# Optimization experiments

Measured on AMD Instinct MI355X. Metric: run time of the kernel, lower is better.

Reference implementation:

```python
import jax, jax.numpy as jnp
import numpy as np

D_MODEL = 1024
N_HEADS = 16
HEAD_DIM = D_MODEL // N_HEADS
LN_EPS = 1e-5


def _linear_init(key, fan_in, fan_out):
    # xavier_uniform for weight, zeros for bias; torch Linear weight is [out, in]
    limit = float(np.sqrt(6.0 / (fan_in + fan_out)))
    w = jax.random.uniform(key, (fan_out, fan_in), jnp.float32, -limit, limit)
    b = jnp.zeros((fan_out,), jnp.float32)
    return w, b


def setup_inputs() -> dict:
    key = jax.random.key(0)
    ks = jax.random.split(key, 8)
    B, S, D = 4, 1024, D_MODEL
    query = jax.random.normal(ks[0], (B, S, D), jnp.float32)
    key_t = jax.random.normal(ks[1], (B, S, D), jnp.float32)
    value = jax.random.normal(ks[2], (B, S, D), jnp.float32)
    Wq, bq = _linear_init(ks[3], D, D)
    Wk, bk = _linear_init(ks[4], D, D)
    Wv, bv = _linear_init(ks[5], D, D)
    Wfq, bfq = _linear_init(ks[6], D, D)
    Wfk, bfk = _linear_init(ks[7], D, D)
    gamma_q = jnp.ones((D,), jnp.float32); beta_q = jnp.zeros((D,), jnp.float32)
    gamma_k = jnp.ones((D,), jnp.float32); beta_k = jnp.zeros((D,), jnp.float32)
    return {"query": query, "key": key_t, "value": value,
            "Wq": Wq, "bq": bq, "Wk": Wk, "bk": bk, "Wv": Wv, "bv": bv,
            "Wfq": Wfq, "bfq": bfq, "Wfk": Wfk, "bfk": bfk,
            "gamma_q": gamma_q, "beta_q": beta_q,
            "gamma_k": gamma_k, "beta_k": beta_k}


def _layernorm(x, gamma, beta):
    mu = jnp.mean(x, axis=-1, keepdims=True)
    var = jnp.mean(jnp.square(x - mu), axis=-1, keepdims=True)
    return (x - mu) * jax.lax.rsqrt(var + LN_EPS) * gamma + beta


def reference(query, key, value, Wq, bq, Wk, bk, Wv, bv, Wfq, bfq, Wfk, bfk,
              gamma_q, beta_q, gamma_k, beta_k):
    B, Sq, D = query.shape
    H, Hd = N_HEADS, HEAD_DIM
    scale = jnp.sqrt(jnp.asarray(Hd, jnp.float32))

    residual_q, residual_k = query, key
    # torch Linear: x @ W.T + b
    q = (query @ Wq.T + bq).reshape(B, Sq, H, Hd).transpose(0, 2, 1, 3)  # [B,H,Sq,Hd]
    k = (key @ Wk.T + bk).reshape(B, -1, H, Hd).transpose(0, 2, 1, 3)    # [B,H,Sk,Hd]
    v = (value @ Wv.T + bv).reshape(B, -1, H, Hd).transpose(0, 2, 1, 3)  # [B,H,Sv,Hd]

    # Q->K attention (dropout disabled / eval mode)
    energy = jnp.einsum('bhqd,bhkd->bhqk', q, k) / scale
    attn_q2k = jax.nn.softmax(energy, axis=-1)
    x_q = jnp.einsum('bhqk,bhkd->bhqd', attn_q2k, v)
    x_q = x_q.transpose(0, 2, 1, 3).reshape(B, Sq, D)

    # K->Q attention (shares V)
    energy_k = jnp.einsum('bhkd,bhqd->bhkq', k, q) / scale
    attn_k2q = jax.nn.softmax(energy_k, axis=-1)
    x_k = jnp.einsum('bhkq,bhqd->bhkd', attn_k2q, v)
    x_k = x_k.transpose(0, 2, 1, 3).reshape(B, -1, D)

    q_out = x_q @ Wfq.T + bfq
    query_out = _layernorm(residual_q + q_out, gamma_q, beta_q)
    k_out = x_k @ Wfk.T + bfk
    key_out = _layernorm(residual_k + k_out, gamma_k, beta_k)
    return (query_out, key_out)
```

## Files before the change

kernel.cpp:

```cpp
#include <hip/hip_runtime.h>

typedef unsigned short u16;
typedef unsigned int u32;
typedef __attribute__((ext_vector_type(8))) short short8;
typedef __attribute__((ext_vector_type(4))) float floatx4;
typedef __attribute__((ext_vector_type(16))) float f32x16;

#define AS_GLOBAL __attribute__((address_space(1)))
#define AS_LDS    __attribute__((address_space(3)))

__device__ __forceinline__ float b2f(u16 v) {
  union { u32 u; float f; } x; x.u = ((u32)v) << 16; return x.f;
}
__device__ __forceinline__ u16 f2bf(float f) {
  union { float f; u32 u; } x; x.f = f;
  u32 r = (x.u + 0x7fffu + ((x.u >> 16) & 1u)) >> 16;
  return (u16)r;
}
__device__ __forceinline__ void gl_lds16(const u16* g, u16* l) {
  __builtin_amdgcn_global_load_lds((const AS_GLOBAL u32*)g, (AS_LDS u32*)l, 16, 0, 0);
}

__global__ __launch_bounds__(256)
void cvt8(const float* __restrict__ s0, const float* __restrict__ s1, const float* __restrict__ s2,
          const float* __restrict__ s3, const float* __restrict__ s4, const float* __restrict__ s5,
          const float* __restrict__ s6, const float* __restrict__ s7,
          u16* __restrict__ d0, u16* __restrict__ d1, u16* __restrict__ d2,
          u16* __restrict__ d3, u16* __restrict__ d4, u16* __restrict__ d5,
          u16* __restrict__ d6, u16* __restrict__ d7, int nbig, int nsmall)
{
  const int z = blockIdx.y;
  const float* s; u16* d; int n;
  switch (z) {
    case 0: s = s0; d = d0; n = nbig; break;
    case 1: s = s1; d = d1; n = nbig; break;
    case 2: s = s2; d = d2; n = nbig; break;
    case 3: s = s3; d = d3; n = nsmall; break;
    case 4: s = s4; d = d4; n = nsmall; break;
    case 5: s = s5; d = d5; n = nsmall; break;
    case 6: s = s6; d = d6; n = nsmall; break;
    default: s = s7; d = d7; n = nsmall; break;
  }
  const size_t idx = ((size_t)blockIdx.x * 256 + threadIdx.x) * 8;
  if (idx >= (size_t)n) return;
  float4 a0 = *(const float4*)(s + idx);
  float4 a1 = *(const float4*)(s + idx + 4);
  u16 t[8];
  t[0] = f2bf(a0.x); t[1] = f2bf(a0.y); t[2] = f2bf(a0.z); t[3] = f2bf(a0.w);
  t[4] = f2bf(a1.x); t[5] = f2bf(a1.y); t[6] = f2bf(a1.z); t[7] = f2bf(a1.w);
  *(uint4*)(d + idx) = *(const uint4*)t;
}

template <int TRANS2>
__global__ __launch_bounds__(256, 3)
void gemm_nt_bias(const u16* __restrict__ A0, const u16* __restrict__ W0, const float* __restrict__ B0, u16* __restrict__ C0,
                  const u16* __restrict__ A1, const u16* __restrict__ W1, const float* __restrict__ B1, u16* __restrict__ C1,
                  const u16* __restrict__ A2, const u16* __restrict__ W2, const float* __restrict__ B2, u16* __restrict__ C2)
{
  constexpr int K = 1024, N = 1024;
  __shared__ __attribute__((aligned(16))) u16 As[128 * 64];
  __shared__ __attribute__((aligned(16))) u16 Bs[128 * 64];

  const int z = blockIdx.z;
  const u16*   A  = z == 0 ? A0 : (z == 1 ? A1 : A2);
  const u16*   W  = z == 0 ? W0 : (z == 1 ? W1 : W2);
  const float* Bi = z == 0 ? B0 : (z == 1 ? B1 : B2);
  u16*         C  = z == 0 ? C0 : (z == 1 ? C1 : C2);

  const int tid  = threadIdx.x;
  const int lane = tid & 63;
  const int wave = tid >> 6;
  const int l16  = lane & 15;
  const int quad = lane >> 4;
  const int wm = wave >> 1, wn = wave & 1;
  const int m0 = blockIdx.x * 128;
  const int n0 = blockIdx.y * 128;

  floatx4 acc[4][4];
#pragma unroll
  for (int i = 0; i < 4; ++i)
#pragma unroll
    for (int j = 0; j < 4; ++j)
#pragma unroll
      for (int e = 0; e < 4; ++e) acc[i][j][e] = 0.f;

  const int srow = wave * 32 + (lane >> 3);
  const int scol = (lane & 7) * 8;
  const u16* gA = A + (size_t)(m0 + srow) * K + scol;
  const u16* gW = W + (size_t)(n0 + srow) * K + scol;

  for (int k0 = 0; k0 < K; k0 += 64) {
#pragma unroll
    for (int i = 0; i < 4; ++i) {
      gl_lds16(gA + (size_t)(i * 8) * K + k0, &As[(wave * 32 + i * 8) * 64]);
      gl_lds16(gW + (size_t)(i * 8) * K + k0, &Bs[(wave * 32 + i * 8) * 64]);
    }
    __syncthreads();
#pragma unroll
    for (int ks = 0; ks < 2; ++ks) {
      short8 af[4], bf[4];
#pragma unroll
      for (int mt = 0; mt < 4; ++mt)
        af[mt] = *(const short8*)&As[(wm * 64 + mt * 16 + l16) * 64 + ks * 32 + quad * 8];
#pragma unroll
      for (int nt = 0; nt < 4; ++nt)
        bf[nt] = *(const short8*)&Bs[(wn * 64 + nt * 16 + l16) * 64 + ks * 32 + quad * 8];
#pragma unroll
      for (int mt = 0; mt < 4; ++mt)
#pragma unroll
        for (int nt = 0; nt < 4; ++nt)
          acc[mt][nt] = __builtin_amdgcn_mfma_f32_16x16x32_bf16(af[mt], bf[nt], acc[mt][nt], 0, 0, 0);
    }
    __syncthreads();
  }

  float bb[4];
#pragma unroll
  for (int nt = 0; nt < 4; ++nt) bb[nt] = Bi[n0 + wn * 64 + nt * 16 + l16];

  if (TRANS2 && z == 2) {
#pragma unroll
    for (int mt = 0; mt < 4; ++mt) {
      const int rowb = m0 + wm * 64 + mt * 16 + quad * 4;
#pragma unroll
      for (int nt = 0; nt < 4; ++nt) {
        const int col = n0 + wn * 64 + nt * 16 + l16;
        u32 lo = (u32)f2bf(acc[mt][nt][0] + bb[nt]) | ((u32)f2bf(acc[mt][nt][1] + bb[nt]) << 16);
        u32 hi = (u32)f2bf(acc[mt][nt][2] + bb[nt]) | ((u32)f2bf(acc[mt][nt][3] + bb[nt]) << 16);
        uint2 w; w.x = lo; w.y = hi;
        *(uint2*)&C[(size_t)col * 4096 + rowb] = w;
      }
    }
  } else {
#pragma unroll
    for (int mt = 0; mt < 4; ++mt) {
#pragma unroll
      for (int r = 0; r < 4; ++r) {
        const int row = m0 + wm * 64 + mt * 16 + quad * 4 + r;
        u16* crow = C + (size_t)row * N + n0 + wn * 64 + l16;
#pragma unroll
        for (int nt = 0; nt < 4; ++nt)
          crow[nt * 16] = f2bf(acc[mt][nt][r] + bb[nt]);
      }
    }
  }
}

__global__ __launch_bounds__(256, 3)
void flash32(const u16* __restrict__ Qg, const u16* __restrict__ Kg,
             const u16* __restrict__ VTw, u16* __restrict__ OQ, u16* __restrict__ OK)
{
  __shared__ __attribute__((aligned(16))) u16 smem[4 * 4096];
  __shared__ __attribute__((aligned(16))) u16 pbuf[4][32 * 64];

  const int tid = threadIdx.x;
  const int lane = tid & 63;
  const int wave = tid >> 6;
  const int l32 = lane & 31;
  const int hi = lane >> 5;
  const int b = blockIdx.y >> 4, h = blockIdx.y & 15;
  const int q0 = blockIdx.x * 128;

  const u16* Qw = blockIdx.z ? Kg : Qg;
  const u16* Kw = blockIdx.z ? Qg : Kg;
  u16* Ow = blockIdx.z ? OK : OQ;

  const int rr = lane >> 3;
  const int s7 = lane & 7;

  const u16* Qt = Qw + ((size_t)(b * 1024 + q0)) * 1024 + h * 64;
  const u16* Kt = Kw + ((size_t)(b * 1024)) * 1024 + h * 64;
  const u16* Vt = VTw + ((size_t)(h * 64)) * 4096 + (size_t)b * 1024;

#pragma unroll
  for (int c = 0; c < 4; ++c) {
    const int R = wave * 32 + c * 8;
    const int cg = ((s7 ^ rr ^ (R >> 3)) & 7) << 3;
    gl_lds16(Qt + (size_t)(R + rr) * 1024 + cg, smem + (R < 64 ? 4096 : 8192) + R * 64);
  }
  {
    u16* kd = smem + wave * 1024;
    u16* vd = smem + 8192 + wave * 1024;
    const int R0 = wave * 16, R1 = wave * 16 + 8;
    const int cg0 = ((s7 ^ rr ^ (R0 >> 3)) & 7) << 3;
    const int cg1 = ((s7 ^ rr ^ (R1 >> 3)) & 7) << 3;
    gl_lds16(Kt + (size_t)(R0 + rr) * 1024 + cg0, kd);
    gl_lds16(Kt + (size_t)(R1 + rr) * 1024 + cg1, kd + 512);
    gl_lds16(Vt + (size_t)(R0 + rr) * 4096 + cg0, vd);
    gl_lds16(Vt + (size_t)(R1 + rr) * 4096 + cg1, vd + 512);
  }
  __syncthreads();

  const int qr = wave * 32 + l32;
  const int qkey = (qr ^ (qr >> 3)) & 7;
  const u16* qbase = smem + (wave < 2 ? 4096 : 8192) + qr * 64;
  short8 aq[4];
#pragma unroll
  for (int d2 = 0; d2 < 4; ++d2)
    aq[d2] = *(const short8*)(qbase + (((d2 * 2 + hi) ^ qkey) & 7) * 8);
  __syncthreads();

  const int key0 = (l32 ^ (l32 >> 3)) & 7;
  const int key1 = key0 ^ 4;

  f32x16 accO0, accO1;
#pragma unroll
  for (int i = 0; i < 16; ++i) { accO0[i] = 0.f; accO1[i] = 0.f; }
  float m = -1e30f, lsum = 0.f;
  const float scale = 0.125f;
  u16* pb = pbuf[wave];

  for (int jt = 0; jt < 16; ++jt) {
    const int cur = jt & 1;
    const u16* ksb = smem + cur * 4096;
    const u16* vtb = smem + 8192 + cur * 4096;

    if (jt + 1 < 16) {
      const int nb = cur ^ 1;
      u16* kd = smem + nb * 4096 + wave * 1024;
      u16* vd = smem + 8192 + nb * 4096 + wave * 1024;
      const int R0 = wave * 16, R1 = wave * 16 + 8;
      const int cg0 = ((s7 ^ rr ^ (R0 >> 3)) & 7) << 3;
      const int cg1 = ((s7 ^ rr ^ (R1 >> 3)) & 7) << 3;
      const size_t tkn = (size_t)((jt + 1) * 64);
      gl_lds16(Kt + (tkn + R0 + rr) * 1024 + cg0, kd);
      gl_lds16(Kt + (tkn + R1 + rr) * 1024 + cg1, kd + 512);
      gl_lds16(Vt + (size_t)(R0 + rr) * 4096 + tkn + cg0, vd);
      gl_lds16(Vt + (size_t)(R1 + rr) * 4096 + tkn + cg1, vd + 512);
    }

    f32x16 s0, s1;
#pragma unroll
    for (int i = 0; i < 16; ++i) { s0[i] = 0.f; s1[i] = 0.f; }
#pragma unroll
    for (int d2 = 0; d2 < 4; ++d2) {
      const int g = d2 * 2 + hi;
      short8 k0 = *(const short8*)(ksb + l32 * 64 + ((g ^ key0) & 7) * 8);
      short8 k1 = *(const short8*)(ksb + (32 + l32) * 64 + ((g ^ key1) & 7) * 8);
      s0 = __builtin_amdgcn_mfma_f32_32x32x16_bf16(k0, aq[d2], s0, 0, 0, 0);
      s1 = __builtin_amdgcn_mfma_f32_32x32x16_bf16(k1, aq[d2], s1, 0, 0, 0);
    }

#define MAX8(v, o) fmaxf(fmaxf(fmaxf(v[o], v[o + 1]), fmaxf(v[o + 2], v[o + 3])), \
                         fmaxf(fmaxf(v[o + 4], v[o + 5]), fmaxf(v[o + 6], v[o + 7])))
#define SUM8(v, o) (((v[o] + v[o + 1]) + (v[o + 2] + v[o + 3])) + \
                    ((v[o + 4] + v[o + 5]) + (v[o + 6] + v[o + 7])))
    float mx = fmaxf(fmaxf(MAX8(s0, 0), MAX8(s0, 8)), fmaxf(MAX8(s1, 0), MAX8(s1, 8)));
    mx = fmaxf(mx, __shfl_xor(mx, 32, 64));
    const float mnew = fmaxf(m, mx * scale);
    const float alpha = __expf(m - mnew);
    m = mnew;
#pragma unroll
    for (int i = 0; i < 16; ++i) s0[i] = __expf(fmaf(s0[i], scale, -mnew));
#pragma unroll
    for (int i = 0; i < 16; ++i) s1[i] = __expf(fmaf(s1[i], scale, -mnew));
    float ssum = (SUM8(s0, 0) + SUM8(s0, 8)) + (SUM8(s1, 0) + SUM8(s1, 8));
    ssum += __shfl_xor(ssum, 32, 64);
    lsum = lsum * alpha + ssum;
#pragma unroll
    for (int i = 0; i < 16; ++i) { accO0[i] *= alpha; accO1[i] *= alpha; }

#define PWRITE(SV, KB)                                                         \
  _Pragma("unroll") for (int rq = 0; rq < 4; ++rq) {                           \
    const int g = (KB) * 4 + rq;                                               \
    uint2 w;                                                                   \
    w.x = (u32)f2bf(SV[rq * 4 + 0]) | ((u32)f2bf(SV[rq * 4 + 1]) << 16);       \
    w.y = (u32)f2bf(SV[rq * 4 + 2]) | ((u32)f2bf(SV[rq * 4 + 3]) << 16);       \
    *(uint2*)&pb[l32 * 64 + ((g ^ key0) & 7) * 8 + hi * 4] = w;                \
  }
    PWRITE(s0, 0)
    PWRITE(s1, 1)
#undef PWRITE

#pragma unroll
    for (int ks = 0; ks < 4; ++ks) {
      const int g = ks * 2 + hi;
      short8 v0 = *(const short8*)(vtb + l32 * 64 + ((g ^ key0) & 7) * 8);
      short8 v1 = *(const short8*)(vtb + (32 + l32) * 64 + ((g ^ key1) & 7) * 8);
      short8 pf = *(const short8*)&pb[l32 * 64 + ((g ^ key0) & 7) * 8];
      accO0 = __builtin_amdgcn_mfma_f32_32x32x16_bf16(v0, pf, accO0, 0, 0, 0);
      accO1 = __builtin_amdgcn_mfma_f32_32x32x16_bf16(v1, pf, accO1, 0, 0, 0);
    }
#undef MAX8
#undef SUM8
    __syncthreads();
  }

  const float invl = 1.f / lsum;
  u16* orow = Ow + ((size_t)(b * 1024 + q0 + wave * 32 + l32)) * 1024 + h * 64 + hi * 4;
#pragma unroll
  for (int rg = 0; rg < 4; ++rg) {
    uint2 w0, w1;
    w0.x = (u32)f2bf(accO0[rg * 4 + 0] * invl) | ((u32)f2bf(accO0[rg * 4 + 1] * invl) << 16);
    w0.y = (u32)f2bf(accO0[rg * 4 + 2] * invl) | ((u32)f2bf(accO0[rg * 4 + 3] * invl) << 16);
    *(uint2*)(orow + rg * 8) = w0;
    w1.x = (u32)f2bf(accO1[rg * 4 + 0] * invl) | ((u32)f2bf(accO1[rg * 4 + 1] * invl) << 16);
    w1.y = (u32)f2bf(accO1[rg * 4 + 2] * invl) | ((u32)f2bf(accO1[rg * 4 + 3] * invl) << 16);
    *(uint2*)(orow + 32 + rg * 8) = w1;
  }
}

__global__ __launch_bounds__(256)
void ln_residual(const u16* __restrict__ TQ, const u16* __restrict__ TK,
                 const float* __restrict__ Rq, const float* __restrict__ Rk,
                 const float* __restrict__ gq, const float* __restrict__ bq,
                 const float* __restrict__ gk, const float* __restrict__ bk,
                 float* __restrict__ out)
{
  const int row = blockIdx.x;
  const u16 *X; const float *R, *G, *Bt; float* O;
  if (row < 4096) {
    X = TQ + (size_t)row * 1024; R = Rq + (size_t)row * 1024;
    G = gq; Bt = bq; O = out + (size_t)row * 1024;
  } else {
    const int r2 = row - 4096;
    X = TK + (size_t)r2 * 1024; R = Rk + (size_t)r2 * 1024;
    G = gk; Bt = bk; O = out + (size_t)4096 * 1024 + (size_t)r2 * 1024;
  }
  const int tid = threadIdx.x;
  float v[4], sum = 0.f, sumsq = 0.f;
#pragma unroll
  for (int i = 0; i < 4; ++i) {
    const int c = tid + i * 256;
    const float x = b2f(X[c]) + R[c];
    v[i] = x; sum += x; sumsq += x * x;
  }
#pragma unroll
  for (int sh = 1; sh < 64; sh <<= 1) {
    sum += __shfl_xor(sum, sh, 64);
    sumsq += __shfl_xor(sumsq, sh, 64);
  }
  __shared__ float sm[8];
  const int wave = tid >> 6, lane = tid & 63;
  if (lane == 0) { sm[wave] = sum; sm[4 + wave] = sumsq; }
  __syncthreads();
  sum = sm[0] + sm[1] + sm[2] + sm[3];
  sumsq = sm[4] + sm[5] + sm[6] + sm[7];
  const float mu = sum * (1.f / 1024.f);
  const float var = sumsq * (1.f / 1024.f) - mu * mu;
  const float rstd = rsqrtf(var + 1e-5f);
#pragma unroll
  for (int i = 0; i < 4; ++i) {
    const int c = tid + i * 256;
    O[c] = (v[i] - mu) * rstd * G[c] + Bt[c];
  }
}

extern "C" void kernel_launch(void* const* d_in, const int* in_sizes, int n_in,
                              void* d_out, int out_size, void* d_ws, size_t ws_size,
                              hipStream_t stream)
{
  const float* query = (const float*)d_in[0];
  const float* key   = (const float*)d_in[1];
  const float* value = (const float*)d_in[2];
  const float* Wq  = (const float*)d_in[3];  const float* bq  = (const float*)d_in[4];
  const float* Wk  = (const float*)d_in[5];  const float* bk  = (const float*)d_in[6];
  const float* Wv  = (const float*)d_in[7];  const float* bv  = (const float*)d_in[8];
  const float* Wfq = (const float*)d_in[9];  const float* bfq = (const float*)d_in[10];
  const float* Wfk = (const float*)d_in[11]; const float* bfk = (const float*)d_in[12];
  const float* gq = (const float*)d_in[13];  const float* betaq = (const float*)d_in[14];
  const float* gk = (const float*)d_in[15];  const float* betak = (const float*)d_in[16];
  float* out = (float*)d_out;
  u16* ws  = (u16*)d_ws;

  const size_t SZ = (size_t)4096 * 1024;
  const size_t WZ = (size_t)1024 * 1024;
  u16* Qb  = ws;
  u16* Kb  = ws + SZ;
  u16* VT  = ws + 2 * SZ;
  u16* Wqb = ws + 3 * SZ;
  u16* Wkb = Wqb + WZ;
  u16* Wvb = Wkb + WZ;
  u16* Wfqb = Wvb + WZ;
  u16* Wfkb = Wfqb + WZ;
  u16* qbf = (u16*)out;
  u16* kbf = qbf + SZ;
  u16* vbf = kbf + SZ;
  u16* XQ = (u16*)out;
  u16* XK = (u16*)out + SZ;
  u16* TQ = Qb;
  u16* TK = Kb;

  cvt8<<<dim3(2048, 8), 256, 0, stream>>>(query, key, value, Wq, Wk, Wv, Wfq, Wfk,
                                          qbf, kbf, vbf, Wqb, Wkb, Wvb, Wfqb, Wfkb,
                                          (int)SZ, (int)WZ);
  gemm_nt_bias<1><<<dim3(32, 8, 3), 256, 0, stream>>>(qbf, Wqb, bq, Qb,
                                                      kbf, Wkb, bk, Kb,
                                                      vbf, Wvb, bv, VT);
  flash32<<<dim3(8, 64, 2), 256, 0, stream>>>(Qb, Kb, VT, XQ, XK);
  gemm_nt_bias<0><<<dim3(32, 8, 2), 256, 0, stream>>>(XQ, Wfqb, bfq, TQ,
                                                      XK, Wfkb, bfk, TK,
                                                      XK, Wfkb, bfk, TK);
  ln_residual<<<dim3(8192), 256, 0, stream>>>(TQ, TK, query, key,
                                              gq, betaq, gk, betak, out);
}
```

Baseline: 283.8 us.

## Rework flash attention softmax: exp2, lazy rescale, split P buffer, occupancy 4

The flash attention kernel gets several changes at once. It uses exp2 with a folded log2e scale and skips the output rescale when the running max grows by less than a threshold. The P tile is written and consumed in two 32-column halves, which halves the P buffer in LDS. It also raises the launch bound to 4 blocks per SM, adds s_setprio around the MFMA blocks, uses packed bf16 conversion intrinsics, and remaps block indices so neighbouring blocks are spread across heads and batches. The aim is less VALU and LDS pressure and higher occupancy, at the risk of register spilling under the tighter bound.

```diff
diff --git a/kernel.cpp b/kernel.cpp
--- a/kernel.cpp
+++ b/kernel.cpp
@@ -1,4 +1,5 @@
 #include <hip/hip_runtime.h>
+#include <hip/hip_bf16.h>
 
 typedef unsigned short u16;
 typedef unsigned int u32;
@@ -16,6 +17,10 @@
   union { float f; u32 u; } x; x.f = f;
   u32 r = (x.u + 0x7fffu + ((x.u >> 16) & 1u)) >> 16;
   return (u16)r;
+}
+__device__ __forceinline__ u32 pk2(float lo, float hi) {
+  __hip_bfloat162 h = __float22bfloat162_rn(make_float2(lo, hi));
+  u32 r; __builtin_memcpy(&r, &h, 4); return r;
 }
 __device__ __forceinline__ void gl_lds16(const u16* g, u16* l) {
   __builtin_amdgcn_global_load_lds((const AS_GLOBAL u32*)g, (AS_LDS u32*)l, 16, 0, 0);
@@ -146,24 +151,30 @@
   }
 }
 
-__global__ __launch_bounds__(256, 3)
+__global__ __launch_bounds__(256, 4)
 void flash32(const u16* __restrict__ Qg, const u16* __restrict__ Kg,
              const u16* __restrict__ VTw, u16* __restrict__ OQ, u16* __restrict__ OK)
 {
   __shared__ __attribute__((aligned(16))) u16 smem[4 * 4096];
-  __shared__ __attribute__((aligned(16))) u16 pbuf[4][32 * 64];
+  __shared__ __attribute__((aligned(16))) u16 pbuf[4][32 * 32];
 
   const int tid = threadIdx.x;
   const int lane = tid & 63;
   const int wave = tid >> 6;
   const int l32 = lane & 31;
   const int hi = lane >> 5;
-  const int b = blockIdx.y >> 4, h = blockIdx.y & 15;
-  const int q0 = blockIdx.x * 128;
-
-  const u16* Qw = blockIdx.z ? Kg : Qg;
-  const u16* Kw = blockIdx.z ? Qg : Kg;
-  u16* Ow = blockIdx.z ? OK : OQ;
+
+  const int jlin = blockIdx.x + 8 * (blockIdx.y + 64 * blockIdx.z);
+  const int L = (jlin & 7) * 128 + (jlin >> 3);
+  const int qx = L & 7;
+  const int by = (L >> 3) & 63;
+  const int bz = L >> 9;
+  const int b = by >> 4, h = by & 15;
+  const int q0 = qx * 128;
+
+  const u16* Qw = bz ? Kg : Qg;
+  const u16* Kw = bz ? Qg : Kg;
+  u16* Ow = bz ? OK : OQ;
 
   const int rr = lane >> 3;
   const int s7 = lane & 7;
@@ -202,13 +213,14 @@
 
   const int key0 = (l32 ^ (l32 >> 3)) & 7;
   const int key1 = key0 ^ 4;
+  const int kq = (l32 >> 2) & 3;
+  u16* pb = pbuf[wave];
 
   f32x16 accO0, accO1;
 #pragma unroll
   for (int i = 0; i < 16; ++i) { accO0[i] = 0.f; accO1[i] = 0.f; }
-  float m = -1e30f, lsum = 0.f;
-  const float scale = 0.125f;
-  u16* pb = pbuf[wave];
+  float m2 = -1e30f, lsum = 0.f;
+  const float SCL2 = 0.18033688011112042f;
 
   for (int jt = 0; jt < 16; ++jt) {
     const int cur = jt & 1;
@@ -232,6 +244,7 @@
     f32x16 s0, s1;
 #pragma unroll
     for (int i = 0; i < 16; ++i) { s0[i] = 0.f; s1[i] = 0.f; }
+    __builtin_amdgcn_s_setprio(1);
 #pragma unroll
     for (int d2 = 0; d2 < 4; ++d2) {
       const int g = d2 * 2 + hi;
@@ -240,6 +253,7 @@
       s0 = __builtin_amdgcn_mfma_f32_32x32x16_bf16(k0, aq[d2], s0, 0, 0, 0);
       s1 = __builtin_amdgcn_mfma_f32_32x32x16_bf16(k1, aq[d2], s1, 0, 0, 0);
     }
+    __builtin_amdgcn_s_setprio(0);
 
 #define MAX8(v, o) fmaxf(fmaxf(fmaxf(v[o], v[o + 1]), fmaxf(v[o + 2], v[o + 3])), \
                          fmaxf(fmaxf(v[o + 4], v[o + 5]), fmaxf(v[o + 6], v[o + 7])))
@@ -247,42 +261,45 @@
                     ((v[o + 4] + v[o + 5]) + (v[o + 6] + v[o + 7])))
     float mx = fmaxf(fmaxf(MAX8(s0, 0), MAX8(s0, 8)), fmaxf(MAX8(s1, 0), MAX8(s1, 8)));
     mx = fmaxf(mx, __shfl_xor(mx, 32, 64));
-    const float mnew = fmaxf(m, mx * scale);
-    const float alpha = __expf(m - mnew);
-    m = mnew;
-#pragma unroll
-    for (int i = 0; i < 16; ++i) s0[i] = __expf(fmaf(s0[i], scale, -mnew));
-#pragma unroll
-    for (int i = 0; i < 16; ++i) s1[i] = __expf(fmaf(s1[i], scale, -mnew));
+    const float mx2 = mx * SCL2;
+    if (!__all(mx2 <= m2 + 8.f)) {
+      const float mnew2 = fmaxf(m2, mx2);
+      const float alpha = exp2f(m2 - mnew2);
+      m2 = mnew2;
+      lsum *= alpha;
+#pragma unroll
+      for (int i = 0; i < 16; ++i) { accO0[i] *= alpha; accO1[i] *= alpha; }
+    }
+#pragma unroll
+    for (int i = 0; i < 16; ++i) s0[i] = exp2f(fmaf(s0[i], SCL2, -m2));
+#pragma unroll
+    for (int i = 0; i < 16; ++i) s1[i] = exp2f(fmaf(s1[i], SCL2, -m2));
     float ssum = (SUM8(s0, 0) + SUM8(s0, 8)) + (SUM8(s1, 0) + SUM8(s1, 8));
     ssum += __shfl_xor(ssum, 32, 64);
-    lsum = lsum * alpha + ssum;
-#pragma unroll
-    for (int i = 0; i < 16; ++i) { accO0[i] *= alpha; accO1[i] *= alpha; }
-
-#define PWRITE(SV, KB)                                                         \
-  _Pragma("unroll") for (int rq = 0; rq < 4; ++rq) {                           \
-    const int g = (KB) * 4 + rq;                                               \
-    uint2 w;                                                                   \
-    w.x = (u32)f2bf(SV[rq * 4 + 0]) | ((u32)f2bf(SV[rq * 4 + 1]) << 16);       \
-    w.y = (u32)f2bf(SV[rq * 4 + 2]) | ((u32)f2bf(SV[rq * 4 + 3]) << 16);       \
-    *(uint2*)&pb[l32 * 64 + ((g ^ key0) & 7) * 8 + hi * 4] = w;                \
-  }
-    PWRITE(s0, 0)
-    PWRITE(s1, 1)
-#undef PWRITE
-
-#pragma unroll
-    for (int ks = 0; ks < 4; ++ks) {
-      const int g = ks * 2 + hi;
-      short8 v0 = *(const short8*)(vtb + l32 * 64 + ((g ^ key0) & 7) * 8);
-      short8 v1 = *(const short8*)(vtb + (32 + l32) * 64 + ((g ^ key1) & 7) * 8);
-      short8 pf = *(const short8*)&pb[l32 * 64 + ((g ^ key0) & 7) * 8];
-      accO0 = __builtin_amdgcn_mfma_f32_32x32x16_bf16(v0, pf, accO0, 0, 0, 0);
-      accO1 = __builtin_amdgcn_mfma_f32_32x32x16_bf16(v1, pf, accO1, 0, 0, 0);
-    }
+    lsum += ssum;
 #undef MAX8
 #undef SUM8
+
+#define PHALF(SV, KB)                                                              \
+    _Pragma("unroll") for (int rq = 0; rq < 4; ++rq) {                             \
+      uint2 w;                                                                     \
+      w.x = pk2(SV[rq * 4 + 0], SV[rq * 4 + 1]);                                   \
+      w.y = pk2(SV[rq * 4 + 2], SV[rq * 4 + 3]);                                   \
+      *(uint2*)&pb[l32 * 32 + ((rq ^ kq) & 3) * 8 + hi * 4] = w;                   \
+    }                                                                              \
+    _Pragma("unroll") for (int kk = 0; kk < 2; ++kk) {                             \
+      const int gv = ((KB) * 2 + kk) * 2 + hi;                                     \
+      short8 v0 = *(const short8*)(vtb + l32 * 64 + ((gv ^ key0) & 7) * 8);        \
+      short8 v1 = *(const short8*)(vtb + (32 + l32) * 64 + ((gv ^ key1) & 7) * 8); \
+      short8 pf = *(const short8*)&pb[l32 * 32 + (((kk * 2 + hi) ^ kq) & 3) * 8];  \
+      __builtin_amdgcn_s_setprio(1);                                               \
+      accO0 = __builtin_amdgcn_mfma_f32_32x32x16_bf16(v0, pf, accO0, 0, 0, 0);     \
+      accO1 = __builtin_amdgcn_mfma_f32_32x32x16_bf16(v1, pf, accO1, 0, 0, 0);     \
+      __builtin_amdgcn_s_setprio(0);                                               \
+    }
+    PHALF(s0, 0)
+    PHALF(s1, 1)
+#undef PHALF
     __syncthreads();
   }
 
@@ -291,11 +308,11 @@
 #pragma unroll
   for (int rg = 0; rg < 4; ++rg) {
     uint2 w0, w1;
-    w0.x = (u32)f2bf(accO0[rg * 4 + 0] * invl) | ((u32)f2bf(accO0[rg * 4 + 1] * invl) << 16);
-    w0.y = (u32)f2bf(accO0[rg * 4 + 2] * invl) | ((u32)f2bf(accO0[rg * 4 + 3] * invl) << 16);
+    w0.x = pk2(accO0[rg * 4 + 0] * invl, accO0[rg * 4 + 1] * invl);
+    w0.y = pk2(accO0[rg * 4 + 2] * invl, accO0[rg * 4 + 3] * invl);
     *(uint2*)(orow + rg * 8) = w0;
-    w1.x = (u32)f2bf(accO1[rg * 4 + 0] * invl) | ((u32)f2bf(accO1[rg * 4 + 1] * invl) << 16);
-    w1.y = (u32)f2bf(accO1[rg * 4 + 2] * invl) | ((u32)f2bf(accO1[rg * 4 + 3] * invl) << 16);
+    w1.x = pk2(accO1[rg * 4 + 0] * invl, accO1[rg * 4 + 1] * invl);
+    w1.y = pk2(accO1[rg * 4 + 2] * invl, accO1[rg * 4 + 3] * invl);
     *(uint2*)(orow + 32 + rg * 8) = w1;
   }
 }
```

After: 284.6 us. About the same (+0.3%).
